# Optimization experiments

Hardware: AMD Instinct MI355X
Metric: run time of the kernel (lower is better)

## Reference

```python
import jax, jax.numpy as jnp
import numpy as np

B, S, D, N, K, NB = 4, 16, 1024, 2, 8, 4
DN = D * N
VOCAB = 151936
VTH_MIN = 0.1
EPS = 1e-6


def _spike(x):
    # Heaviside forward, sigmoid surrogate (alpha=4) backward (spikingjelly default)
    sur = jax.nn.sigmoid(4.0 * x)
    return sur + jax.lax.stop_gradient((x >= 0.0).astype(x.dtype) - sur)


def setup_inputs() -> dict:
    key = jax.random.key(0)
    ks = jax.random.split(key, 16)
    def w(k, shape, fan_in):
        return jax.random.normal(k, shape, jnp.float32) * np.float32(1.0 / np.sqrt(fan_in))
    return {
        "token_ids": jax.random.randint(ks[0], (B, S), 0, VOCAB),
        "embed": jax.random.normal(ks[1], (VOCAB, D), jnp.float32) * 0.02,
        "norm_w": jnp.ones((D,), jnp.float32),
        "enc_W": w(ks[2], (D, D), D), "enc_b": jnp.zeros((D,), jnp.float32),
        "dec_W": w(ks[3], (D, D), D), "dec_b": jnp.zeros((D,), jnp.float32),
        "Win": w(ks[4], (NB, DN, D), D),
        "WbX": w(ks[5], (NB, DN, D), D),
        "WaX": w(ks[6], (NB, DN, D), D),
        "WtX": w(ks[7], (NB, DN, D), D),
        "WbV": w(ks[8], (NB, DN, DN), DN),
        "WaV": w(ks[9], (NB, DN, DN), DN),
        "WtV": w(ks[10], (NB, DN, DN), DN),
        "b_beta": jnp.zeros((NB, DN), jnp.float32),
        "b_alpha": jnp.zeros((NB, DN), jnp.float32),
        "b_th": jnp.zeros((NB, DN), jnp.float32),
        "Wgate": w(ks[11], (NB, D, D), D),
        "Wskip": w(ks[12], (NB, D, D), D),
        "Wout": w(ks[13], (NB, D, DN), DN),
        "plif_w": jnp.zeros((NB,), jnp.float32),  # sigmoid(0)=0.5 -> tau=2
        "out_vth": jnp.array([0.3] + [0.05] * (NB - 1), jnp.float32),
    }


def _forward(token_ids, embed, norm_w, enc_W, enc_b, dec_W, dec_b,
             Win, WbX, WaX, WtX, WbV, WaV, WtV,
             b_beta, b_alpha, b_th, Wgate, Wskip, Wout, plif_w, out_vth):
    bit_w = 2.0 ** (-jnp.arange(1, K + 1, dtype=jnp.float32))  # MSB-first weights

    def block_step(i, x, V, u):
        # x: (B, D) spikes; V: (B, DN) membrane state; u: (B, D) output-neuron state
        beta = jax.nn.sigmoid(x @ WbX[i].T + V @ WbV[i].T + b_beta[i])
        alpha = jax.nn.sigmoid(x @ WaX[i].T + V @ WaV[i].T + b_alpha[i])
        vth = VTH_MIN + jax.nn.softplus(x @ WtX[i].T + V @ WtV[i].T + b_th[i])
        V = beta * V + alpha * (x @ Win[i].T)
        sp = _spike(V - vth)
        V = V - sp * vth  # soft reset
        cur = jax.nn.sigmoid(x @ Wgate[i].T) * (sp @ Wout[i].T) + x @ Wskip[i].T
        u = u + (cur - u) * jax.nn.sigmoid(plif_w[i])  # PLIF dynamics
        so = _spike(u - out_vth[i])
        u = (1.0 - so) * u  # hard reset to 0
        return so, V, u

    def token_step(state, ids_t):
        Vs, us = state
        emb = embed[ids_t]                                  # (B, D)
        h = jax.nn.sigmoid(emb @ enc_W.T + enc_b)
        def enc(res, _):
            bit = (res >= 0.5).astype(res.dtype)
            return (res - 0.5 * bit) * 2.0, bit
        _, frames = jax.lax.scan(enc, h, None, length=K)    # (K, B, D) binary
        def kstep(st, frame):
            Vs, us = st
            s = frame
            nV, nu = [], []
            for i in range(NB):
                s, vi, ui = block_step(i, s, Vs[i], us[i])
                nV.append(vi); nu.append(ui)
            return (jnp.stack(nV), jnp.stack(nu)), s
        (Vs, us), out_frames = jax.lax.scan(kstep, (Vs, us), frames)
        decoded = jnp.einsum('kbd,k->bd', out_frames, bit_w)
        hh = decoded @ dec_W.T + dec_b
        var = jnp.mean(hh * hh, axis=-1, keepdims=True)
        hh = norm_w * (hh * jax.lax.rsqrt(var + EPS))       # RMSNorm
        logits = hh @ embed.T                               # tied lm head, (B, VOCAB)
        return (Vs, us), logits

    V0 = jnp.zeros((NB, B, DN), jnp.float32)
    u0 = jnp.zeros((NB, B, D), jnp.float32)
    _, logits = jax.lax.scan(token_step, (V0, u0), token_ids.T)  # (S, B, VOCAB)
    return jnp.transpose(logits, (1, 0, 2))


def reference(token_ids, embed, norm_w, enc_W, enc_b, dec_W, dec_b,
              Win, WbX, WaX, WtX, WbV, WaV, WtV,
              b_beta, b_alpha, b_th, Wgate, Wskip, Wout, plif_w, out_vth):
    return _forward(token_ids, embed, norm_w, enc_W, enc_b, dec_W, dec_b,
                    Win, WbX, WaX, WtX, WbV, WaV, WtV,
                    b_beta, b_alpha, b_th, Wgate, Wskip, Wout, plif_w, out_vth)
```

## Files before the change

kernel.cpp:

```cpp
#include <hip/hip_runtime.h>

constexpr int B = 4, S = 16, D = 1024, DN = 2048, NB = 4, K = 8, VOCAB = 151936;

__device__ __forceinline__ float sigf(float x) { return 1.0f / (1.0f + expf(-x)); }
__device__ __forceinline__ float softplusf(float x) {
  return fmaxf(x, 0.0f) + log1pf(expf(-fabsf(x)));
}

template<int N>
__device__ __forceinline__ void wred(float* a) {
#pragma unroll
  for (int m = 1; m < 64; m <<= 1) {
#pragma unroll
    for (int q = 0; q < N; ++q) a[q] += __shfl_xor(a[q], m, 64);
  }
}

__global__ __launch_bounds__(256) void enc_kernel(
    const int* __restrict__ token_ids, int t,
    const float* __restrict__ embed, const float* __restrict__ enc_W,
    const float* __restrict__ enc_b, float* __restrict__ h_out) {
  __shared__ float sE[B * D];
  for (int idx = threadIdx.x; idx < (B * D) / 4; idx += 256) {
    int b = idx / (D / 4);
    int c = idx % (D / 4);
    int id = token_ids[b * S + t];
    ((float4*)sE)[idx] = ((const float4*)(embed + (size_t)id * D))[c];
  }
  __syncthreads();
  const int lane = threadIdx.x & 63;
  const int d = (blockIdx.x << 2) + (threadIdx.x >> 6);
  float a[4] = {0.f, 0.f, 0.f, 0.f};
  const float4* wrow = (const float4*)(enc_W + (size_t)d * D);
  for (int c = lane; c < D / 4; c += 64) {
    float4 w = wrow[c];
#pragma unroll
    for (int b = 0; b < 4; ++b) {
      float4 sv = ((const float4*)(sE + b * D))[c];
      a[b] = fmaf(w.x, sv.x, fmaf(w.y, sv.y, fmaf(w.z, sv.z, fmaf(w.w, sv.w, a[b]))));
    }
  }
  wred<4>(a);
  if (lane == 0) {
    float eb = enc_b[d];
#pragma unroll
    for (int b = 0; b < 4; ++b) h_out[b * D + d] = sigf(a[b] + eb);
  }
}

__global__ __launch_bounds__(256) void bits_kernel(const float* __restrict__ h,
                                                   float* __restrict__ frames) {
  int idx = blockIdx.x * 256 + threadIdx.x;
  if (idx >= B * D) return;
  float res = h[idx];
#pragma unroll
  for (int k = 0; k < K; ++k) {
    float bit = (res >= 0.5f) ? 1.0f : 0.0f;
    frames[k * B * D + idx] = bit;
    res = (res - 0.5f * bit) * 2.0f;
  }
}

__global__ __launch_bounds__(256) void phase1_kernel(
    const float* __restrict__ s_in,
    const float* __restrict__ Vread,
    float* __restrict__ Vwrite,
    float* __restrict__ sp_out,
    const float* __restrict__ WbX, const float* __restrict__ WaX,
    const float* __restrict__ WtX, const float* __restrict__ Win,
    const float* __restrict__ WbV, const float* __restrict__ WaV,
    const float* __restrict__ WtV,
    const float* __restrict__ bb_, const float* __restrict__ ba_,
    const float* __restrict__ bt_) {
  __shared__ float sS[B * D];
  __shared__ float sV[B * DN];
  for (int idx = threadIdx.x; idx < (B * D) / 4; idx += 256)
    ((float4*)sS)[idx] = ((const float4*)s_in)[idx];
  for (int idx = threadIdx.x; idx < (B * DN) / 4; idx += 256)
    ((float4*)sV)[idx] = ((const float4*)Vread)[idx];
  __syncthreads();

  const int lane = threadIdx.x & 63;
  const int j = (blockIdx.x << 2) + (threadIdx.x >> 6);

  float acc[16];
#pragma unroll
  for (int q = 0; q < 16; ++q) acc[q] = 0.f;

  const float4* wbx = (const float4*)(WbX + (size_t)j * D);
  const float4* wax = (const float4*)(WaX + (size_t)j * D);
  const float4* wtx = (const float4*)(WtX + (size_t)j * D);
  const float4* win = (const float4*)(Win + (size_t)j * D);
  for (int c = lane; c < D / 4; c += 64) {
    float4 wb = wbx[c], wa = wax[c], wt = wtx[c], wi = win[c];
#pragma unroll
    for (int b = 0; b < 4; ++b) {
      float4 sv = ((const float4*)(sS + b * D))[c];
      acc[0 + b]  = fmaf(wb.x, sv.x, fmaf(wb.y, sv.y, fmaf(wb.z, sv.z, fmaf(wb.w, sv.w, acc[0 + b]))));
      acc[4 + b]  = fmaf(wa.x, sv.x, fmaf(wa.y, sv.y, fmaf(wa.z, sv.z, fmaf(wa.w, sv.w, acc[4 + b]))));
      acc[8 + b]  = fmaf(wt.x, sv.x, fmaf(wt.y, sv.y, fmaf(wt.z, sv.z, fmaf(wt.w, sv.w, acc[8 + b]))));
      acc[12 + b] = fmaf(wi.x, sv.x, fmaf(wi.y, sv.y, fmaf(wi.z, sv.z, fmaf(wi.w, sv.w, acc[12 + b]))));
    }
  }

  const float4* wbv = (const float4*)(WbV + (size_t)j * DN);
  const float4* wav = (const float4*)(WaV + (size_t)j * DN);
  const float4* wtv = (const float4*)(WtV + (size_t)j * DN);
  for (int c = lane; c < DN / 4; c += 64) {
    float4 wb = wbv[c], wa = wav[c], wt = wtv[c];
#pragma unroll
    for (int b = 0; b < 4; ++b) {
      float4 vv = ((const float4*)(sV + b * DN))[c];
      acc[0 + b] = fmaf(wb.x, vv.x, fmaf(wb.y, vv.y, fmaf(wb.z, vv.z, fmaf(wb.w, vv.w, acc[0 + b]))));
      acc[4 + b] = fmaf(wa.x, vv.x, fmaf(wa.y, vv.y, fmaf(wa.z, vv.z, fmaf(wa.w, vv.w, acc[4 + b]))));
      acc[8 + b] = fmaf(wt.x, vv.x, fmaf(wt.y, vv.y, fmaf(wt.z, vv.z, fmaf(wt.w, vv.w, acc[8 + b]))));
    }
  }

  wred<16>(acc);

  if (lane == 0) {
    float bb = bb_[j], ba = ba_[j], bt = bt_[j];
#pragma unroll
    for (int b = 0; b < 4; ++b) {
      float beta = sigf(acc[0 + b] + bb);
      float alpha = sigf(acc[4 + b] + ba);
      float vth = 0.1f + softplusf(acc[8 + b] + bt);
      float Vold = sV[b * DN + j];
      float Vn = beta * Vold + alpha * acc[12 + b];
      float spike = (Vn - vth >= 0.0f) ? 1.0f : 0.0f;
      Vn = Vn - spike * vth;
      Vwrite[b * DN + j] = Vn;
      sp_out[b * DN + j] = spike;
    }
  }
}

__global__ __launch_bounds__(256) void phase2_kernel(
    const float* __restrict__ s_in,
    const float* __restrict__ sp_in,
    float* __restrict__ u,
    float* __restrict__ so_out,
    const float* __restrict__ Wgate, const float* __restrict__ Wskip,
    const float* __restrict__ Wout,
    const float* __restrict__ plif_p, const float* __restrict__ vth_p) {
  __shared__ float sS[B * D];
  __shared__ float sP[B * DN];
  for (int idx = threadIdx.x; idx < (B * D) / 4; idx += 256)
    ((float4*)sS)[idx] = ((const float4*)s_in)[idx];
  for (int idx = threadIdx.x; idx < (B * DN) / 4; idx += 256)
    ((float4*)sP)[idx] = ((const float4*)sp_in)[idx];
  __syncthreads();

  const int lane = threadIdx.x & 63;
  const int d = (blockIdx.x << 2) + (threadIdx.x >> 6);

  float acc[12];
#pragma unroll
  for (int q = 0; q < 12; ++q) acc[q] = 0.f;

  const float4* wg = (const float4*)(Wgate + (size_t)d * D);
  const float4* wk = (const float4*)(Wskip + (size_t)d * D);
  for (int c = lane; c < D / 4; c += 64) {
    float4 g = wg[c], k = wk[c];
#pragma unroll
    for (int b = 0; b < 4; ++b) {
      float4 sv = ((const float4*)(sS + b * D))[c];
      acc[0 + b] = fmaf(g.x, sv.x, fmaf(g.y, sv.y, fmaf(g.z, sv.z, fmaf(g.w, sv.w, acc[0 + b]))));
      acc[4 + b] = fmaf(k.x, sv.x, fmaf(k.y, sv.y, fmaf(k.z, sv.z, fmaf(k.w, sv.w, acc[4 + b]))));
    }
  }
  const float4* wo = (const float4*)(Wout + (size_t)d * DN);
  for (int c = lane; c < DN / 4; c += 64) {
    float4 o = wo[c];
#pragma unroll
    for (int b = 0; b < 4; ++b) {
      float4 pv = ((const float4*)(sP + b * DN))[c];
      acc[8 + b] = fmaf(o.x, pv.x, fmaf(o.y, pv.y, fmaf(o.z, pv.z, fmaf(o.w, pv.w, acc[8 + b]))));
    }
  }

  wred<12>(acc);

  if (lane == 0) {
    float pl = sigf(plif_p[0]);
    float ovth = vth_p[0];
#pragma unroll
    for (int b = 0; b < 4; ++b) {
      float g = sigf(acc[0 + b]);
      float cur = fmaf(g, acc[8 + b], acc[4 + b]);
      float uo = u[b * D + d];
      float un = uo + (cur - uo) * pl;
      float so = (un - ovth >= 0.0f) ? 1.0f : 0.0f;
      u[b * D + d] = (1.0f - so) * un;
      so_out[b * D + d] = so;
    }
  }
}

__global__ __launch_bounds__(256) void decode_kernel(const float* __restrict__ outf,
                                                     float* __restrict__ decoded) {
  int idx = blockIdx.x * 256 + threadIdx.x;
  int t = idx / (B * D);
  int rem = idx % (B * D);
  float acc = 0.f, w = 0.5f;
#pragma unroll
  for (int k = 0; k < K; ++k) {
    acc = fmaf(outf[(size_t)(t * K + k) * B * D + rem], w, acc);
    w *= 0.5f;
  }
  decoded[idx] = acc;
}

__global__ __launch_bounds__(256) void decgemm_kernel(
    const float* __restrict__ decoded,
    const float* __restrict__ dec_W,
    const float* __restrict__ dec_b, float* __restrict__ hh_pre) {
  __shared__ float sDec[16 * D];
  const int g = blockIdx.x & 3;
  for (int idx = threadIdx.x; idx < (16 * D) / 4; idx += 256)
    ((float4*)sDec)[idx] = ((const float4*)(decoded + (size_t)g * 16 * D))[idx];
  __syncthreads();

  const int lane = threadIdx.x & 63;
  const int d = (blockIdx.x >> 2) * 4 + (threadIdx.x >> 6);
  float acc[16];
#pragma unroll
  for (int q = 0; q < 16; ++q) acc[q] = 0.f;
  const float4* wrow = (const float4*)(dec_W + (size_t)d * D);
  for (int c = lane; c < D / 4; c += 64) {
    float4 w = wrow[c];
#pragma unroll
    for (int r = 0; r < 16; ++r) {
      float4 x = ((const float4*)(sDec + r * D))[c];
      acc[r] = fmaf(w.x, x.x, fmaf(w.y, x.y, fmaf(w.z, x.z, fmaf(w.w, x.w, acc[r]))));
    }
  }
  wred<16>(acc);
  if (lane == 0) {
    float bb = dec_b[d];
#pragma unroll
    for (int r = 0; r < 16; ++r) hh_pre[(size_t)(g * 16 + r) * D + d] = acc[r] + bb;
  }
}

__global__ __launch_bounds__(256) void rmsnorm_kernel(const float* __restrict__ hh_pre,
                                                      const float* __restrict__ norm_w,
                                                      float* __restrict__ hh) {
  const int r = blockIdx.x;
  const int lane = threadIdx.x & 63, w = threadIdx.x >> 6;
  __shared__ float red[4];
  float ss = 0.f;
  for (int d = threadIdx.x; d < D; d += 256) {
    float v = hh_pre[(size_t)r * D + d];
    ss = fmaf(v, v, ss);
  }
#pragma unroll
  for (int m = 1; m < 64; m <<= 1) ss += __shfl_xor(ss, m, 64);
  if (lane == 0) red[w] = ss;
  __syncthreads();
  float tot = red[0] + red[1] + red[2] + red[3];
  float scale = rsqrtf(tot * (1.0f / D) + 1e-6f);
  for (int d = threadIdx.x; d < D; d += 256)
    hh[(size_t)r * D + d] = norm_w[d] * (hh_pre[(size_t)r * D + d] * scale);
}

__device__ __forceinline__ unsigned int bf16rn(float f) {
  unsigned int x = __float_as_uint(f);
  return (x + 0x7fffu + ((x >> 16) & 1u)) >> 16;
}

__global__ __launch_bounds__(256) void lmhead_kernel(
    const float* __restrict__ hh,
    const float* __restrict__ embed,
    float* __restrict__ out) {
  __shared__ unsigned int sH[(D / 4) * 64];
  const int half = blockIdx.x & 1;
  const int vblk = blockIdx.x >> 1;
  const int d0 = half * (D / 2);
  for (int e = threadIdx.x; e < (D / 4) * 64; e += 256) {
    int d2 = e >> 6, r = e & 63;
    float f0 = hh[(size_t)r * D + d0 + 2 * d2];
    float f1 = hh[(size_t)r * D + d0 + 2 * d2 + 1];
    sH[e] = bf16rn(f0) | (bf16rn(f1) << 16);
  }
  __syncthreads();

  const int lane = threadIdx.x & 63;
  const int wave = (vblk << 2) + (threadIdx.x >> 6);
  for (int v = wave; v < VOCAB; v += 1024) {
    const float4* erow = (const float4*)(embed + (size_t)v * D + d0);
    float acc = 0.f;
#pragma unroll 4
    for (int c = 0; c < (D / 2) / 4; ++c) {
      float4 e4 = erow[c];
      unsigned int p0 = sH[(c * 2) * 64 + lane];
      unsigned int p1 = sH[(c * 2 + 1) * 64 + lane];
      float h0 = __uint_as_float(p0 << 16);
      float h1 = __uint_as_float(p0 & 0xffff0000u);
      float h2 = __uint_as_float(p1 << 16);
      float h3 = __uint_as_float(p1 & 0xffff0000u);
      acc = fmaf(e4.x, h0, fmaf(e4.y, h1, fmaf(e4.z, h2, fmaf(e4.w, h3, acc))));
    }
    int tt = lane >> 2, b = lane & 3;
    atomicAdd(&out[((size_t)b * S + tt) * VOCAB + v], acc);
  }
}

extern "C" void kernel_launch(void* const* d_in, const int* in_sizes, int n_in,
                              void* d_out, int out_size, void* d_ws, size_t ws_size,
                              hipStream_t stream) {
  const int* token_ids = (const int*)d_in[0];
  const float* embed   = (const float*)d_in[1];
  const float* norm_w  = (const float*)d_in[2];
  const float* enc_W   = (const float*)d_in[3];
  const float* enc_b   = (const float*)d_in[4];
  const float* dec_W   = (const float*)d_in[5];
  const float* dec_b   = (const float*)d_in[6];
  const float* Win     = (const float*)d_in[7];
  const float* WbX     = (const float*)d_in[8];
  const float* WaX     = (const float*)d_in[9];
  const float* WtX     = (const float*)d_in[10];
  const float* WbV     = (const float*)d_in[11];
  const float* WaV     = (const float*)d_in[12];
  const float* WtV     = (const float*)d_in[13];
  const float* b_beta  = (const float*)d_in[14];
  const float* b_alpha = (const float*)d_in[15];
  const float* b_th    = (const float*)d_in[16];
  const float* Wgate   = (const float*)d_in[17];
  const float* Wskip   = (const float*)d_in[18];
  const float* Wout    = (const float*)d_in[19];
  const float* plif_w  = (const float*)d_in[20];
  const float* out_vth = (const float*)d_in[21];

  float* ws = (float*)d_ws;
  float* frames  = ws;
  float* Vbuf    = frames + K * B * D;
  float* u       = Vbuf + 2 * NB * B * DN;
  float* sp      = u + NB * B * D;
  float* so      = sp + B * DN;
  float* outf    = so + NB * B * D;
  float* h       = outf + S * K * B * D;
  float* decoded = h + B * D;
  float* hh_pre  = decoded + S * B * D;
  float* hh      = hh_pre + S * B * D;

  hipMemsetAsync(Vbuf, 0, (size_t)NB * B * DN * sizeof(float), stream);
  hipMemsetAsync(u, 0, (size_t)NB * B * D * sizeof(float), stream);
  hipMemsetAsync(d_out, 0, (size_t)out_size * sizeof(float), stream);

  for (int t = 0; t < S; ++t) {
    enc_kernel<<<256, 256, 0, stream>>>(token_ids, t, embed, enc_W, enc_b, h);
    bits_kernel<<<16, 256, 0, stream>>>(h, frames);
    for (int k = 0; k < K; ++k) {
      int p = (t * K + k) & 1;
      const float* s_cur = frames + (size_t)k * B * D;
      for (int i = 0; i < NB; ++i) {
        const float* Vr = Vbuf + (size_t)p * NB * B * DN + (size_t)i * B * DN;
        float* Vw = Vbuf + (size_t)(1 - p) * NB * B * DN + (size_t)i * B * DN;
        phase1_kernel<<<512, 256, 0, stream>>>(
            s_cur, Vr, Vw, sp,
            WbX + (size_t)i * DN * D, WaX + (size_t)i * DN * D,
            WtX + (size_t)i * DN * D, Win + (size_t)i * DN * D,
            WbV + (size_t)i * DN * DN, WaV + (size_t)i * DN * DN,
            WtV + (size_t)i * DN * DN,
            b_beta + i * DN, b_alpha + i * DN, b_th + i * DN);
        float* dest = (i < NB - 1) ? (so + (size_t)i * B * D)
                                   : (outf + (size_t)(t * K + k) * B * D);
        phase2_kernel<<<256, 256, 0, stream>>>(
            s_cur, sp, u + (size_t)i * B * D, dest,
            Wgate + (size_t)i * D * D, Wskip + (size_t)i * D * D,
            Wout + (size_t)i * D * DN, plif_w + i, out_vth + i);
        s_cur = dest;
      }
    }
  }
  decode_kernel<<<(S * B * D) / 256, 256, 0, stream>>>(outf, decoded);
  decgemm_kernel<<<1024, 256, 0, stream>>>(decoded, dec_W, dec_b, hh_pre);
  rmsnorm_kernel<<<S * B, 256, 0, stream>>>(hh_pre, norm_w, hh);
  lmhead_kernel<<<512, 256, 0, stream>>>(hh, embed, (float*)d_out);
}
```

Before: 21.43 ms.

## Fuse recurrent SNN loop into one persistent cooperative kernel with grid barriers

Replaces the roughly thousand per-step phase1/phase2 launches, plus the encoder and bit-split kernels, with a single persistent cooperative kernel that synchronises through a hierarchical atomic grid barrier. The V-dependent gate products (WbV/WaV/WtV) for the next block are precomputed one step ahead and spread across phase 1 and phase 2, so phase 2 no longer leaves half the waves idle. Decoding is folded into the loop as a running sum. This removes launch overhead and balances the work, at the cost of spin-wait barriers and a forward-progress risk if the grid is not fully co-resident.

```diff
diff --git a/kernel.cpp b/kernel.cpp
--- a/kernel.cpp
+++ b/kernel.cpp
@@ -1,13 +1,18 @@
 #include <hip/hip_runtime.h>
 
 constexpr int B = 4, S = 16, D = 1024, DN = 2048, NB = 4, K = 8, VOCAB = 151936;
+constexpr int NSTEP = S * K * NB;
+constexpr int NBLK = 512;
 
 __device__ __forceinline__ float sigf(float x) { return 1.0f / (1.0f + expf(-x)); }
 __device__ __forceinline__ float softplusf(float x) {
   return fmaxf(x, 0.0f) + log1pf(expf(-fabsf(x)));
 }
-
-template<int N>
+__device__ __forceinline__ float dot4(float4 w, float4 v, float a) {
+  return fmaf(w.x, v.x, fmaf(w.y, v.y, fmaf(w.z, v.z, fmaf(w.w, v.w, a))));
+}
+
+template <int N>
 __device__ __forceinline__ void wred(float* a) {
 #pragma unroll
   for (int m = 1; m < 64; m <<= 1) {
@@ -16,200 +21,259 @@
   }
 }
 
-__global__ __launch_bounds__(256) void enc_kernel(
-    const int* __restrict__ token_ids, int t,
-    const float* __restrict__ embed, const float* __restrict__ enc_W,
-    const float* __restrict__ enc_b, float* __restrict__ h_out) {
-  __shared__ float sE[B * D];
-  for (int idx = threadIdx.x; idx < (B * D) / 4; idx += 256) {
-    int b = idx / (D / 4);
-    int c = idx % (D / 4);
-    int id = token_ids[b * S + t];
-    ((float4*)sE)[idx] = ((const float4*)(embed + (size_t)id * D))[c];
-  }
+__device__ __forceinline__ void gbar(int* bar, int epoch) {
   __syncthreads();
-  const int lane = threadIdx.x & 63;
-  const int d = (blockIdx.x << 2) + (threadIdx.x >> 6);
-  float a[4] = {0.f, 0.f, 0.f, 0.f};
-  const float4* wrow = (const float4*)(enc_W + (size_t)d * D);
-  for (int c = lane; c < D / 4; c += 64) {
-    float4 w = wrow[c];
-#pragma unroll
-    for (int b = 0; b < 4; ++b) {
-      float4 sv = ((const float4*)(sE + b * D))[c];
-      a[b] = fmaf(w.x, sv.x, fmaf(w.y, sv.y, fmaf(w.z, sv.z, fmaf(w.w, sv.w, a[b]))));
-    }
-  }
-  wred<4>(a);
-  if (lane == 0) {
-    float eb = enc_b[d];
-#pragma unroll
-    for (int b = 0; b < 4; ++b) h_out[b * D + d] = sigf(a[b] + eb);
-  }
-}
-
-__global__ __launch_bounds__(256) void bits_kernel(const float* __restrict__ h,
-                                                   float* __restrict__ frames) {
-  int idx = blockIdx.x * 256 + threadIdx.x;
-  if (idx >= B * D) return;
-  float res = h[idx];
-#pragma unroll
-  for (int k = 0; k < K; ++k) {
-    float bit = (res >= 0.5f) ? 1.0f : 0.0f;
-    frames[k * B * D + idx] = bit;
-    res = (res - 0.5f * bit) * 2.0f;
-  }
-}
-
-__global__ __launch_bounds__(256) void phase1_kernel(
-    const float* __restrict__ s_in,
-    const float* __restrict__ Vread,
-    float* __restrict__ Vwrite,
-    float* __restrict__ sp_out,
-    const float* __restrict__ WbX, const float* __restrict__ WaX,
-    const float* __restrict__ WtX, const float* __restrict__ Win,
+  if (threadIdx.x == 0) {
+    int* gcnt = bar + 32 + ((blockIdx.x & 63) << 4);
+    int a = __hip_atomic_fetch_add(gcnt, 1, __ATOMIC_ACQ_REL, __HIP_MEMORY_SCOPE_AGENT);
+    if (((a + 1) & 7) == 0) {
+      int r = __hip_atomic_fetch_add(bar, 1, __ATOMIC_ACQ_REL, __HIP_MEMORY_SCOPE_AGENT);
+      if (r + 1 == 64 * epoch)
+        __hip_atomic_store(bar + 16, epoch, __ATOMIC_RELEASE, __HIP_MEMORY_SCOPE_AGENT);
+    }
+    while (__hip_atomic_load(bar + 16, __ATOMIC_RELAXED, __HIP_MEMORY_SCOPE_AGENT) < epoch)
+      __builtin_amdgcn_s_sleep(2);
+    (void)__hip_atomic_load(bar + 16, __ATOMIC_ACQUIRE, __HIP_MEMORY_SCOPE_AGENT);
+  }
+  __syncthreads();
+}
+
+__global__ __launch_bounds__(256, 2) void snn_main(
+    const int* __restrict__ token_ids, const float* __restrict__ embed,
+    const float* __restrict__ enc_W, const float* __restrict__ enc_b,
+    const float* __restrict__ Win, const float* __restrict__ WbX,
+    const float* __restrict__ WaX, const float* __restrict__ WtX,
     const float* __restrict__ WbV, const float* __restrict__ WaV,
     const float* __restrict__ WtV,
-    const float* __restrict__ bb_, const float* __restrict__ ba_,
-    const float* __restrict__ bt_) {
-  __shared__ float sS[B * D];
-  __shared__ float sV[B * DN];
-  for (int idx = threadIdx.x; idx < (B * D) / 4; idx += 256)
-    ((float4*)sS)[idx] = ((const float4*)s_in)[idx];
-  for (int idx = threadIdx.x; idx < (B * DN) / 4; idx += 256)
-    ((float4*)sV)[idx] = ((const float4*)Vread)[idx];
-  __syncthreads();
-
-  const int lane = threadIdx.x & 63;
-  const int j = (blockIdx.x << 2) + (threadIdx.x >> 6);
-
-  float acc[16];
-#pragma unroll
-  for (int q = 0; q < 16; ++q) acc[q] = 0.f;
-
-  const float4* wbx = (const float4*)(WbX + (size_t)j * D);
-  const float4* wax = (const float4*)(WaX + (size_t)j * D);
-  const float4* wtx = (const float4*)(WtX + (size_t)j * D);
-  const float4* win = (const float4*)(Win + (size_t)j * D);
-  for (int c = lane; c < D / 4; c += 64) {
-    float4 wb = wbx[c], wa = wax[c], wt = wtx[c], wi = win[c];
-#pragma unroll
-    for (int b = 0; b < 4; ++b) {
-      float4 sv = ((const float4*)(sS + b * D))[c];
-      acc[0 + b]  = fmaf(wb.x, sv.x, fmaf(wb.y, sv.y, fmaf(wb.z, sv.z, fmaf(wb.w, sv.w, acc[0 + b]))));
-      acc[4 + b]  = fmaf(wa.x, sv.x, fmaf(wa.y, sv.y, fmaf(wa.z, sv.z, fmaf(wa.w, sv.w, acc[4 + b]))));
-      acc[8 + b]  = fmaf(wt.x, sv.x, fmaf(wt.y, sv.y, fmaf(wt.z, sv.z, fmaf(wt.w, sv.w, acc[8 + b]))));
-      acc[12 + b] = fmaf(wi.x, sv.x, fmaf(wi.y, sv.y, fmaf(wi.z, sv.z, fmaf(wi.w, sv.w, acc[12 + b]))));
-    }
-  }
-
-  const float4* wbv = (const float4*)(WbV + (size_t)j * DN);
-  const float4* wav = (const float4*)(WaV + (size_t)j * DN);
-  const float4* wtv = (const float4*)(WtV + (size_t)j * DN);
-  for (int c = lane; c < DN / 4; c += 64) {
-    float4 wb = wbv[c], wa = wav[c], wt = wtv[c];
-#pragma unroll
-    for (int b = 0; b < 4; ++b) {
-      float4 vv = ((const float4*)(sV + b * DN))[c];
-      acc[0 + b] = fmaf(wb.x, vv.x, fmaf(wb.y, vv.y, fmaf(wb.z, vv.z, fmaf(wb.w, vv.w, acc[0 + b]))));
-      acc[4 + b] = fmaf(wa.x, vv.x, fmaf(wa.y, vv.y, fmaf(wa.z, vv.z, fmaf(wa.w, vv.w, acc[4 + b]))));
-      acc[8 + b] = fmaf(wt.x, vv.x, fmaf(wt.y, vv.y, fmaf(wt.z, vv.z, fmaf(wt.w, vv.w, acc[8 + b]))));
-    }
-  }
-
-  wred<16>(acc);
-
-  if (lane == 0) {
-    float bb = bb_[j], ba = ba_[j], bt = bt_[j];
-#pragma unroll
-    for (int b = 0; b < 4; ++b) {
-      float beta = sigf(acc[0 + b] + bb);
-      float alpha = sigf(acc[4 + b] + ba);
-      float vth = 0.1f + softplusf(acc[8 + b] + bt);
-      float Vold = sV[b * DN + j];
-      float Vn = beta * Vold + alpha * acc[12 + b];
-      float spike = (Vn - vth >= 0.0f) ? 1.0f : 0.0f;
-      Vn = Vn - spike * vth;
-      Vwrite[b * DN + j] = Vn;
-      sp_out[b * DN + j] = spike;
-    }
-  }
-}
-
-__global__ __launch_bounds__(256) void phase2_kernel(
-    const float* __restrict__ s_in,
-    const float* __restrict__ sp_in,
-    float* __restrict__ u,
-    float* __restrict__ so_out,
+    const float* __restrict__ b_beta, const float* __restrict__ b_alpha,
+    const float* __restrict__ b_th,
     const float* __restrict__ Wgate, const float* __restrict__ Wskip,
     const float* __restrict__ Wout,
-    const float* __restrict__ plif_p, const float* __restrict__ vth_p) {
-  __shared__ float sS[B * D];
-  __shared__ float sP[B * DN];
-  for (int idx = threadIdx.x; idx < (B * D) / 4; idx += 256)
-    ((float4*)sS)[idx] = ((const float4*)s_in)[idx];
-  for (int idx = threadIdx.x; idx < (B * DN) / 4; idx += 256)
-    ((float4*)sP)[idx] = ((const float4*)sp_in)[idx];
-  __syncthreads();
+    const float* __restrict__ plif_w, const float* __restrict__ out_vth,
+    float* __restrict__ frames, float* __restrict__ sp, float* __restrict__ sbuf,
+    float* __restrict__ V, float* __restrict__ u, float* __restrict__ GV,
+    float* __restrict__ decoded, int* bar) {
+  __shared__ float lds[B * D + B * DN];
+  float* sS = lds;
+  float* sX = lds + B * D;
 
   const int lane = threadIdx.x & 63;
-  const int d = (blockIdx.x << 2) + (threadIdx.x >> 6);
-
-  float acc[12];
-#pragma unroll
-  for (int q = 0; q < 12; ++q) acc[q] = 0.f;
-
-  const float4* wg = (const float4*)(Wgate + (size_t)d * D);
-  const float4* wk = (const float4*)(Wskip + (size_t)d * D);
-  for (int c = lane; c < D / 4; c += 64) {
-    float4 g = wg[c], k = wk[c];
-#pragma unroll
-    for (int b = 0; b < 4; ++b) {
-      float4 sv = ((const float4*)(sS + b * D))[c];
-      acc[0 + b] = fmaf(g.x, sv.x, fmaf(g.y, sv.y, fmaf(g.z, sv.z, fmaf(g.w, sv.w, acc[0 + b]))));
-      acc[4 + b] = fmaf(k.x, sv.x, fmaf(k.y, sv.y, fmaf(k.z, sv.z, fmaf(k.w, sv.w, acc[4 + b]))));
-    }
-  }
-  const float4* wo = (const float4*)(Wout + (size_t)d * DN);
-  for (int c = lane; c < DN / 4; c += 64) {
-    float4 o = wo[c];
-#pragma unroll
-    for (int b = 0; b < 4; ++b) {
-      float4 pv = ((const float4*)(sP + b * DN))[c];
-      acc[8 + b] = fmaf(o.x, pv.x, fmaf(o.y, pv.y, fmaf(o.z, pv.z, fmaf(o.w, pv.w, acc[8 + b]))));
-    }
-  }
-
-  wred<12>(acc);
-
-  if (lane == 0) {
-    float pl = sigf(plif_p[0]);
-    float ovth = vth_p[0];
-#pragma unroll
-    for (int b = 0; b < 4; ++b) {
-      float g = sigf(acc[0 + b]);
-      float cur = fmaf(g, acc[8 + b], acc[4 + b]);
-      float uo = u[b * D + d];
-      float un = uo + (cur - uo) * pl;
-      float so = (un - ovth >= 0.0f) ? 1.0f : 0.0f;
-      u[b * D + d] = (1.0f - so) * un;
-      so_out[b * D + d] = so;
-    }
-  }
-}
-
-__global__ __launch_bounds__(256) void decode_kernel(const float* __restrict__ outf,
-                                                     float* __restrict__ decoded) {
-  int idx = blockIdx.x * 256 + threadIdx.x;
-  int t = idx / (B * D);
-  int rem = idx % (B * D);
-  float acc = 0.f, w = 0.5f;
-#pragma unroll
-  for (int k = 0; k < K; ++k) {
-    acc = fmaf(outf[(size_t)(t * K + k) * B * D + rem], w, acc);
-    w *= 0.5f;
-  }
-  decoded[idx] = acc;
+  const int warp = threadIdx.x >> 6;
+  const int gw = (blockIdx.x << 2) + warp;
+  int epoch = 0;
+
+  {
+    const int d = gw & 1023;
+    const int t0 = gw >> 10;
+    const float4* wrow = (const float4*)(enc_W + (size_t)d * D);
+    for (int rep = 0; rep < 8; ++rep) {
+      const int t = t0 * 8 + rep;
+      float a[4] = {0.f, 0.f, 0.f, 0.f};
+      int ids[4];
+#pragma unroll
+      for (int b = 0; b < 4; ++b) ids[b] = token_ids[b * S + t];
+#pragma unroll
+      for (int c = lane; c < D / 4; c += 64) {
+        float4 w = wrow[c];
+#pragma unroll
+        for (int b = 0; b < 4; ++b) {
+          float4 e = ((const float4*)(embed + (size_t)ids[b] * D))[c];
+          a[b] = dot4(w, e, a[b]);
+        }
+      }
+      wred<4>(a);
+      if (lane == 0) {
+        float eb = enc_b[d];
+#pragma unroll
+        for (int b = 0; b < 4; ++b) {
+          float res = sigf(a[b] + eb);
+#pragma unroll
+          for (int k = 0; k < K; ++k) {
+            float bit = (res >= 0.5f) ? 1.0f : 0.0f;
+            frames[((size_t)(t * K + k) * B + b) * D + d] = bit;
+            res = (res - 0.5f * bit) * 2.0f;
+          }
+        }
+      }
+    }
+  }
+  gbar(bar, ++epoch);
+
+  float dec[4] = {0.f, 0.f, 0.f, 0.f};
+
+  for (int n = 0; n < NSTEP; ++n) {
+    const int i = n & 3;
+    const int kk = (n >> 2) & 7;
+    const int t = n >> 5;
+    const int i2 = (n + 1) & 3;
+    const bool doVU = (n + 1 < NSTEP);
+    const int par_r = n & 1, par_w = par_r ^ 1;
+    const float* s_read = (i == 0) ? frames + (size_t)(t * K + kk) * B * D
+                                   : sbuf + (size_t)(n & 1) * B * D;
+
+    for (int idx = threadIdx.x; idx < (B * D) / 4; idx += 256)
+      ((float4*)sS)[idx] = ((const float4*)s_read)[idx];
+    if (doVU)
+      for (int idx = threadIdx.x; idx < (B * DN) / 4; idx += 256)
+        ((float4*)sX)[idx] = ((const float4*)(V + (size_t)i2 * B * DN))[idx];
+    __syncthreads();
+
+    {
+      const int j = gw;
+      float acc[20];
+#pragma unroll
+      for (int q = 0; q < 20; ++q) acc[q] = 0.f;
+      const float4* wbx = (const float4*)(WbX + ((size_t)i * DN + j) * D);
+      const float4* wax = (const float4*)(WaX + ((size_t)i * DN + j) * D);
+      const float4* wtx = (const float4*)(WtX + ((size_t)i * DN + j) * D);
+      const float4* win = (const float4*)(Win + ((size_t)i * DN + j) * D);
+#pragma unroll
+      for (int c = lane; c < D / 4; c += 64) {
+        float4 wb = wbx[c], wa = wax[c], wt = wtx[c], wi = win[c];
+#pragma unroll
+        for (int b = 0; b < 4; ++b) {
+          float4 sv = ((const float4*)(sS + b * D))[c];
+          acc[0 + b]  = dot4(wb, sv, acc[0 + b]);
+          acc[4 + b]  = dot4(wa, sv, acc[4 + b]);
+          acc[8 + b]  = dot4(wt, sv, acc[8 + b]);
+          acc[12 + b] = dot4(wi, sv, acc[12 + b]);
+        }
+      }
+      if (doVU) {
+        const float4* wbv = (const float4*)(WbV + ((size_t)i2 * DN + j) * DN);
+#pragma unroll
+        for (int c = lane; c < DN / 4; c += 64) {
+          float4 wv = wbv[c];
+#pragma unroll
+          for (int b = 0; b < 4; ++b) {
+            float4 vv = ((const float4*)(sX + b * DN))[c];
+            acc[16 + b] = dot4(wv, vv, acc[16 + b]);
+          }
+        }
+      }
+      wred<20>(acc);
+      if (lane == 0) {
+        const float bb = b_beta[i * DN + j], ba = b_alpha[i * DN + j], bt = b_th[i * DN + j];
+#pragma unroll
+        for (int b = 0; b < 4; ++b) {
+          float gb = GV[((size_t)(par_r * 3 + 0) * B + b) * DN + j];
+          float ga = GV[((size_t)(par_r * 3 + 1) * B + b) * DN + j];
+          float gt = GV[((size_t)(par_r * 3 + 2) * B + b) * DN + j];
+          float beta = sigf(acc[0 + b] + gb + bb);
+          float alpha = sigf(acc[4 + b] + ga + ba);
+          float vth = 0.1f + softplusf(acc[8 + b] + gt + bt);
+          float Vold = V[((size_t)i * B + b) * DN + j];
+          float Vn = beta * Vold + alpha * acc[12 + b];
+          float spike = (Vn - vth >= 0.0f) ? 1.0f : 0.0f;
+          V[((size_t)i * B + b) * DN + j] = Vn - spike * vth;
+          sp[b * DN + j] = spike;
+          if (doVU) GV[((size_t)(par_w * 3 + 0) * B + b) * DN + j] = acc[16 + b];
+        }
+      }
+    }
+    gbar(bar, ++epoch);
+
+    if (gw < 1024) {
+      for (int idx = threadIdx.x; idx < (B * DN) / 4; idx += 256)
+        ((float4*)sX)[idx] = ((const float4*)sp)[idx];
+      __syncthreads();
+      const int d = gw;
+      float acc[16];
+#pragma unroll
+      for (int q = 0; q < 16; ++q) acc[q] = 0.f;
+      const float4* wg = (const float4*)(Wgate + ((size_t)i * D + d) * D);
+      const float4* wk = (const float4*)(Wskip + ((size_t)i * D + d) * D);
+#pragma unroll
+      for (int c = lane; c < D / 4; c += 64) {
+        float4 g = wg[c], k = wk[c];
+#pragma unroll
+        for (int b = 0; b < 4; ++b) {
+          float4 sv = ((const float4*)(sS + b * D))[c];
+          acc[0 + b] = dot4(g, sv, acc[0 + b]);
+          acc[4 + b] = dot4(k, sv, acc[4 + b]);
+        }
+      }
+      const float4* wo = (const float4*)(Wout + ((size_t)i * D + d) * DN);
+#pragma unroll
+      for (int c = lane; c < DN / 4; c += 64) {
+        float4 o = wo[c];
+#pragma unroll
+        for (int b = 0; b < 4; ++b) {
+          float4 pv = ((const float4*)(sX + b * DN))[c];
+          acc[8 + b] = dot4(o, pv, acc[8 + b]);
+        }
+      }
+      if (doVU) {
+        const float4* wav = (const float4*)(WaV + ((size_t)i2 * DN + d) * DN);
+        const float4* vg = (const float4*)(V + (size_t)i2 * B * DN);
+#pragma unroll
+        for (int c = lane; c < DN / 4; c += 64) {
+          float4 wv = wav[c];
+#pragma unroll
+          for (int b = 0; b < 4; ++b) {
+            float4 vv = vg[b * (DN / 4) + c];
+            acc[12 + b] = dot4(wv, vv, acc[12 + b]);
+          }
+        }
+      }
+      wred<16>(acc);
+      if (lane == 0) {
+        float pl = sigf(plif_w[i]);
+        float ovth = out_vth[i];
+        float bw = ldexpf(1.0f, -(kk + 1));
+        float* s_write = sbuf + (size_t)((n + 1) & 1) * B * D;
+#pragma unroll
+        for (int b = 0; b < 4; ++b) {
+          float g = sigf(acc[0 + b]);
+          float cur = fmaf(g, acc[8 + b], acc[4 + b]);
+          float uo = u[((size_t)i * B + b) * D + d];
+          float un = uo + (cur - uo) * pl;
+          float so = (un - ovth >= 0.0f) ? 1.0f : 0.0f;
+          u[((size_t)i * B + b) * D + d] = (1.0f - so) * un;
+          if (i < 3) {
+            s_write[b * D + d] = so;
+          } else {
+            dec[b] = fmaf(so, bw, dec[b]);
+            if (kk == 7) {
+              decoded[((size_t)t * B + b) * D + d] = dec[b];
+              dec[b] = 0.f;
+            }
+          }
+          if (doVU) GV[((size_t)(par_w * 3 + 1) * B + b) * DN + d] = acc[12 + b];
+        }
+      }
+    } else if (doVU) {
+      const int v = gw - 1024;
+      const int ja = 1024 + v;
+      float acc[12];
+#pragma unroll
+      for (int q = 0; q < 12; ++q) acc[q] = 0.f;
+      const float4* w0 = (const float4*)(WaV + ((size_t)i2 * DN + ja) * DN);
+      const float4* w1 = (const float4*)(WtV + ((size_t)i2 * DN + v) * DN);
+      const float4* w2 = (const float4*)(WtV + ((size_t)i2 * DN + ja) * DN);
+#pragma unroll
+      for (int c = lane; c < DN / 4; c += 64) {
+        float4 a0 = w0[c], a1 = w1[c], a2 = w2[c];
+#pragma unroll
+        for (int b = 0; b < 4; ++b) {
+          float4 vv = ((const float4*)(sX + b * DN))[c];
+          acc[0 + b] = dot4(a0, vv, acc[0 + b]);
+          acc[4 + b] = dot4(a1, vv, acc[4 + b]);
+          acc[8 + b] = dot4(a2, vv, acc[8 + b]);
+        }
+      }
+      wred<12>(acc);
+      if (lane == 0) {
+#pragma unroll
+        for (int b = 0; b < 4; ++b) {
+          GV[((size_t)(par_w * 3 + 1) * B + b) * DN + ja] = acc[0 + b];
+          GV[((size_t)(par_w * 3 + 2) * B + b) * DN + v] = acc[4 + b];
+          GV[((size_t)(par_w * 3 + 2) * B + b) * DN + ja] = acc[8 + b];
+        }
+      }
+    }
+    gbar(bar, ++epoch);
+  }
 }
 
 __global__ __launch_bounds__(256) void decgemm_kernel(
@@ -335,47 +399,38 @@
 
   float* ws = (float*)d_ws;
   float* frames  = ws;
-  float* Vbuf    = frames + K * B * D;
-  float* u       = Vbuf + 2 * NB * B * DN;
-  float* sp      = u + NB * B * D;
-  float* so      = sp + B * DN;
-  float* outf    = so + NB * B * D;
-  float* h       = outf + S * K * B * D;
-  float* decoded = h + B * D;
-  float* hh_pre  = decoded + S * B * D;
-  float* hh      = hh_pre + S * B * D;
-
-  hipMemsetAsync(Vbuf, 0, (size_t)NB * B * DN * sizeof(float), stream);
-  hipMemsetAsync(u, 0, (size_t)NB * B * D * sizeof(float), stream);
+  float* sp      = frames + S * K * B * D;
+  float* sbuf    = sp + B * DN;
+  float* V       = sbuf + 2 * B * D;
+  float* u       = V + NB * B * DN;
+  float* GV      = u + NB * B * D;
+  float* decoded = GV + 2 * 3 * B * DN;
+  int*   bar     = (int*)(decoded + S * B * D);
+  float* hh_pre  = frames;
+  float* hh      = frames + S * B * D;
+
+  hipMemsetAsync(V, 0,
+                 (size_t)(NB * B * DN + NB * B * D + 2 * 3 * B * DN + S * B * D) * sizeof(float) +
+                 2048 * sizeof(int), stream);
   hipMemsetAsync(d_out, 0, (size_t)out_size * sizeof(float), stream);
 
-  for (int t = 0; t < S; ++t) {
-    enc_kernel<<<256, 256, 0, stream>>>(token_ids, t, embed, enc_W, enc_b, h);
-    bits_kernel<<<16, 256, 0, stream>>>(h, frames);
-    for (int k = 0; k < K; ++k) {
-      int p = (t * K + k) & 1;
-      const float* s_cur = frames + (size_t)k * B * D;
-      for (int i = 0; i < NB; ++i) {
-        const float* Vr = Vbuf + (size_t)p * NB * B * DN + (size_t)i * B * DN;
-        float* Vw = Vbuf + (size_t)(1 - p) * NB * B * DN + (size_t)i * B * DN;
-        phase1_kernel<<<512, 256, 0, stream>>>(
-            s_cur, Vr, Vw, sp,
-            WbX + (size_t)i * DN * D, WaX + (size_t)i * DN * D,
-            WtX + (size_t)i * DN * D, Win + (size_t)i * DN * D,
-            WbV + (size_t)i * DN * DN, WaV + (size_t)i * DN * DN,
-            WtV + (size_t)i * DN * DN,
-            b_beta + i * DN, b_alpha + i * DN, b_th + i * DN);
-        float* dest = (i < NB - 1) ? (so + (size_t)i * B * D)
-                                   : (outf + (size_t)(t * K + k) * B * D);
-        phase2_kernel<<<256, 256, 0, stream>>>(
-            s_cur, sp, u + (size_t)i * B * D, dest,
-            Wgate + (size_t)i * D * D, Wskip + (size_t)i * D * D,
-            Wout + (size_t)i * D * DN, plif_w + i, out_vth + i);
-        s_cur = dest;
-      }
-    }
-  }
-  decode_kernel<<<(S * B * D) / 256, 256, 0, stream>>>(outf, decoded);
+  void* args[] = {(void*)&token_ids, (void*)&embed, (void*)&enc_W, (void*)&enc_b,
+                  (void*)&Win, (void*)&WbX, (void*)&WaX, (void*)&WtX,
+                  (void*)&WbV, (void*)&WaV, (void*)&WtV,
+                  (void*)&b_beta, (void*)&b_alpha, (void*)&b_th,
+                  (void*)&Wgate, (void*)&Wskip, (void*)&Wout,
+                  (void*)&plif_w, (void*)&out_vth,
+                  (void*)&frames, (void*)&sp, (void*)&sbuf,
+                  (void*)&V, (void*)&u, (void*)&GV, (void*)&decoded, (void*)&bar};
+  hipError_t err = hipLaunchCooperativeKernel((void*)snn_main, dim3(NBLK), dim3(256),
+                                              args, 0, stream);
+  if (err != hipSuccess) {
+    snn_main<<<dim3(NBLK), dim3(256), 0, stream>>>(
+        token_ids, embed, enc_W, enc_b, Win, WbX, WaX, WtX, WbV, WaV, WtV,
+        b_beta, b_alpha, b_th, Wgate, Wskip, Wout, plif_w, out_vth,
+        frames, sp, sbuf, V, u, GV, decoded, bar);
+  }
+
   decgemm_kernel<<<1024, 256, 0, stream>>>(decoded, dec_W, dec_b, hh_pre);
   rmsnorm_kernel<<<S * B, 256, 0, stream>>>(hh_pre, norm_w, hh);
   lmhead_kernel<<<512, 256, 0, stream>>>(hh, embed, (float*)d_out);
```

Measured after the change: 45.18 ms. 2.11x slower.
